# Kernel tuning notes

Measured on AMD Instinct MI355X. Metric: run time of the kernel, lower is better.

The kernel has to match this reference:

```python
import math
import jax, jax.numpy as jnp
import numpy as np

K = 64            # multiplicity per irrep
NE = 10           # num_elements
N_NODES = 10000
N_EDGES = 100000
AVG_NEIGH = 10.0
EDGE_DIM = 8
LS = [0, 1, 2]    # node/intermediate irreps 64x0e+64x1o+64x2e
LS_OUT = [0, 1]   # output irreps 64x0e+64x1o
INV_SQRT_K = 1.0 / math.sqrt(K)
MIX_NORM = 1.0 / math.sqrt(K * NE)

# ---- real spherical-harmonic Clebsch-Gordan coefficients (small l, exact) ----
def _cg(j1, m1, j2, m2, j3, m3):
    if m1 + m2 != m3 or not (abs(j1 - j2) <= j3 <= j1 + j2):
        return 0.0
    f = math.factorial
    pre = math.sqrt((2 * j3 + 1) * f(j1 + j2 - j3) * f(j1 - j2 + j3) * f(-j1 + j2 + j3) / f(j1 + j2 + j3 + 1))
    pre *= math.sqrt(f(j1 + m1) * f(j1 - m1) * f(j2 + m2) * f(j2 - m2) * f(j3 + m3) * f(j3 - m3))
    s = 0.0
    for k in range(j1 + j2 + j3 + 1):
        d = (j1 + j2 - j3 - k, j1 - m1 - k, j2 + m2 - k, j3 - j2 + m1 + k, j3 - j1 - m2 + k)
        if min(d) < 0:
            continue
        s += (-1) ** k / (f(k) * f(d[0]) * f(d[1]) * f(d[2]) * f(d[3]) * f(d[4]))
    return pre * s

def _u_real(l):
    # complex->real SH change of basis: Y_real = U @ Y_complex
    U = np.zeros((2 * l + 1, 2 * l + 1), dtype=np.complex128)
    U[l, l] = 1.0
    s = 1.0 / math.sqrt(2.0)
    for m in range(1, l + 1):
        U[l + m, l + m] = (-1) ** m * s
        U[l + m, l - m] = s
        U[l - m, l + m] = -1j * (-1) ** m * s
        U[l - m, l - m] = 1j * s
    return U

def real_cg(l1, l2, l3):
    C = np.zeros((2 * l1 + 1, 2 * l2 + 1, 2 * l3 + 1), dtype=np.complex128)
    for m1 in range(-l1, l1 + 1):
        for m2 in range(-l2, l2 + 1):
            m3 = m1 + m2
            if abs(m3) <= l3:
                C[l1 + m1, l2 + m2, l3 + m3] = _cg(l1, m1, l2, m2, l3, m3)
    U1, U2, U3 = _u_real(l1), _u_real(l2), _u_real(l3)
    Cr = np.einsum('ai,bj,ck,ijk->abc', U1, U2, U3.conj(), C)
    return np.ascontiguousarray(Cr.real).astype(np.float32)  # real since l1+l2+l3 even

# parity/triangle allowed paths (l1: edge sph, l2: node in, l3: intermediate) -> 11 paths
EDGE_PATHS = [(l1, l2, l3) for l1 in LS for l2 in LS for l3 in LS
              if abs(l1 - l2) <= l3 <= l1 + l2 and (l1 + l2 + l3) % 2 == 0]
N_EDGE_PATHS = len(EDGE_PATHS)  # 11
DEG2_PATHS = [(0, 0, 0), (1, 1, 0), (2, 2, 0), (0, 1, 1), (1, 2, 1)]
DEG3_PATHS = [(0, 0, 0), (1, 1, 0), (0, 1, 1), (1, 0, 1), (1, 2, 1)]
CG_EDGE = [real_cg(*p) for p in EDGE_PATHS]
CG_D2 = [real_cg(*p) for p in DEG2_PATHS]
CG_D3 = [real_cg(*p) for p in DEG3_PATHS]

def split_irreps(x, ls, mul):
    # ir_mul layout: per irrep a [(2l+1)*mul] flat segment, m index outer
    out, o = [], 0
    for l in ls:
        d = (2 * l + 1) * mul
        out.append(x[:, o:o + d].reshape(x.shape[0], 2 * l + 1, mul))
        o += d
    return out


def setup_inputs() -> dict:
    key = jax.random.key(0)
    ks = jax.random.split(key, 20)
    sender = jax.random.randint(ks[0], (N_EDGES,), 0, N_NODES)
    receiver = jax.random.randint(ks[1], (N_EDGES,), 0, N_NODES)
    indices = jax.random.randint(ks[2], (N_NODES,), 0, NE)
    node_attrs = jax.nn.one_hot(indices, NE, dtype=jnp.float32)
    node_feature_in = jax.random.normal(ks[3], (N_NODES, K * 9), dtype=jnp.float32)
    edge_length_embed = jax.random.normal(ks[4], (N_EDGES, EDGE_DIM), dtype=jnp.float32)
    edge_sph_embed = jax.random.normal(ks[5], (N_EDGES, 9), dtype=jnp.float32)
    W_lin_in = jax.random.normal(ks[6], (3, K, K), dtype=jnp.float32)
    mlp_W0 = jax.random.normal(ks[7], (EDGE_DIM, 32), dtype=jnp.float32) / math.sqrt(EDGE_DIM)
    mlp_b0 = jnp.zeros((32,), jnp.float32)
    mlp_W1 = jax.random.normal(ks[8], (32, 32), dtype=jnp.float32) / math.sqrt(32.0)
    mlp_b1 = jnp.zeros((32,), jnp.float32)
    mlp_W2 = jax.random.normal(ks[9], (32, 32), dtype=jnp.float32) / math.sqrt(32.0)
    mlp_b2 = jnp.zeros((32,), jnp.float32)
    mlp_W3 = jax.random.normal(ks[10], (32, N_EDGE_PATHS * K), dtype=jnp.float32) / math.sqrt(32.0)
    mlp_b3 = jnp.zeros((N_EDGE_PATHS * K,), jnp.float32)
    W_mix = jax.random.normal(ks[11], (3, NE, K, K), dtype=jnp.float32)
    w1 = jax.random.normal(ks[12], (NE, 2, K), dtype=jnp.float32)
    w2 = 0.1 * jax.random.normal(ks[13], (NE, len(DEG2_PATHS), K), dtype=jnp.float32)
    w3 = 0.05 * jax.random.normal(ks[14], (NE, len(DEG3_PATHS), K), dtype=jnp.float32)
    W_out_m = jax.random.normal(ks[15], (2, K, K), dtype=jnp.float32)
    W_out_h = jax.random.normal(ks[16], (2, K, K), dtype=jnp.float32)
    return dict(sender=sender, receiver=receiver, indices=indices, node_attrs=node_attrs,
                node_feature_in=node_feature_in, edge_length_embed=edge_length_embed,
                edge_sph_embed=edge_sph_embed, W_lin_in=W_lin_in,
                mlp_W0=mlp_W0, mlp_b0=mlp_b0, mlp_W1=mlp_W1, mlp_b1=mlp_b1,
                mlp_W2=mlp_W2, mlp_b2=mlp_b2, mlp_W3=mlp_W3, mlp_b3=mlp_b3,
                W_mix=W_mix, w1=w1, w2=w2, w3=w3, W_out_m=W_out_m, W_out_h=W_out_h)


def reference(sender, receiver, indices, node_attrs, node_feature_in,
              edge_length_embed, edge_sph_embed, W_lin_in,
              mlp_W0, mlp_b0, mlp_W1, mlp_b1, mlp_W2, mlp_b2, mlp_W3, mlp_b3,
              W_mix, w1, w2, w3, W_out_m, W_out_h):
    N = node_feature_in.shape[0]
    h1 = split_irreps(node_feature_in, LS, K)  # per-l [N, 2l+1, K]
    # ELinear_h1_2_h1p: per-irrep channel mixing
    h1p = [jnp.einsum('nmc,cd->nmd', h1[l], W_lin_in[l]) * INV_SQRT_K for l in LS]
    # residual radial MLP -> per-edge TP path weights [E, P, K]
    h = jax.nn.silu(edge_length_embed @ mlp_W0 + mlp_b0)
    h = h + jax.nn.silu(h @ mlp_W1 + mlp_b1)
    h = h + jax.nn.silu(h @ mlp_W2 + mlp_b2)
    Rl = (h @ mlp_W3 + mlp_b3).reshape(-1, N_EDGE_PATHS, K)
    sph = split_irreps(edge_sph_embed, LS, 1)  # per-l [E, 2l+1, 1]
    gx = [h1p[l][sender] for l in LS]          # gather sender node features
    # channelwise equivariant tensor product with per-edge radial weights
    msg = [None, None, None]
    for p, (l1, l2, l3) in enumerate(EDGE_PATHS):
        t = jnp.einsum('abd,ea,ebc->edc', jnp.asarray(CG_EDGE[p]), sph[l1][:, :, 0], gx[l2])
        t = t * Rl[:, p, None, :]
        msg[l3] = t if msg[l3] is None else msg[l3] + t
    # scatter-sum messages to receivers, normalized by avg num neighbors
    A = [jax.ops.segment_sum(msg[l], receiver, num_segments=N) / AVG_NEIGH for l in LS]
    # element-conditioned mixing (FCTP with num_elements x 0e attrs)
    Amix = [jnp.einsum('nmc,ne,ecd->nmd', A[l], node_attrs, W_mix[l]) * MIX_NORM for l in LS]
    # symmetric contraction (body order 3) with element-dependent channelwise weights
    w1n, w2n, w3n = w1[indices], w2[indices], w3[indices]
    T2 = [jnp.zeros_like(Amix[L]) for L in LS_OUT]
    for p, (l1, l2, L) in enumerate(DEG2_PATHS):
        t = jnp.einsum('abd,nac,nbc->ndc', jnp.asarray(CG_D2[p]), Amix[l1], Amix[l2])
        T2[L] = T2[L] + w2n[:, p, None, :] * t
    T3 = [jnp.zeros_like(Amix[L]) for L in LS_OUT]
    for q, (Lp, l3, L) in enumerate(DEG3_PATHS):
        t = jnp.einsum('abd,nac,nbc->ndc', jnp.asarray(CG_D3[q]), T2[Lp], Amix[l3])
        T3[L] = T3[L] + w3n[:, q, None, :] * t
    B = [w1n[:, L, None, :] * Amix[L] + T2[L] + T3[L] for L in LS_OUT]
    # node_feature_out = ELinear_h1_2_h2(h1) + ELinear_m2_2_h2(B)
    out = []
    for L in LS_OUT:
        y = jnp.einsum('nmc,cd->nmd', h1[L], W_out_h[L]) * INV_SQRT_K
        y = y + jnp.einsum('nmc,cd->nmd', B[L], W_out_m[L]) * INV_SQRT_K
        out.append(y.reshape(N, -1))
    return jnp.concatenate(out, axis=1)  # [N, 4K] = [N, 256]
```

## Files before the change

kernel.cpp:

```cpp
#include <hip/hip_runtime.h>
#include <math.h>

#define NNODES 10000
#define NEDGES 100000

typedef float v2f __attribute__((ext_vector_type(2)));

struct Cplx { double re, im; };

constexpr double cfact(int n){ double r=1.0; for(int i=2;i<=n;++i) r*=i; return r; }

constexpr double csqrt_(double x){
  if (x<=0.0) return 0.0;
  double g = x<1.0 ? 1.0 : x;
  for (int it=0; it<64; ++it){ double ng = 0.5*(g + x/g); if (ng==g) break; g = ng; }
  return g;
}

constexpr double cg_coeff(int j1,int m1,int j2,int m2,int j3,int m3){
  if (m1+m2!=m3) return 0.0;
  int lo = j1>j2 ? j1-j2 : j2-j1;
  if (j3<lo || j3>j1+j2) return 0.0;
  if (m1<-j1||m1>j1||m2<-j2||m2>j2||m3<-j3||m3>j3) return 0.0;
  double pre = csqrt_((2.0*j3+1.0)*cfact(j1+j2-j3)*cfact(j1-j2+j3)*cfact(-j1+j2+j3)/cfact(j1+j2+j3+1));
  pre *= csqrt_(cfact(j1+m1)*cfact(j1-m1)*cfact(j2+m2)*cfact(j2-m2)*cfact(j3+m3)*cfact(j3-m3));
  double s = 0.0;
  for (int k=0;k<=j1+j2+j3;++k){
    int d0=j1+j2-j3-k, d1=j1-m1-k, d2=j2+m2-k, d3=j3-j2+m1+k, d4=j3-j1-m2+k;
    if (d0<0||d1<0||d2<0||d3<0||d4<0) continue;
    double term = 1.0/(cfact(k)*cfact(d0)*cfact(d1)*cfact(d2)*cfact(d3)*cfact(d4));
    s += (k&1) ? -term : term;
  }
  return pre*s;
}

constexpr Cplx uent(int l,int a,int i){
  const double s = 0.70710678118654752440;
  int ma = a - l;
  if (ma==0) { if (i==l) return Cplx{1.0,0.0}; return Cplx{0.0,0.0}; }
  if (ma>0){
    int m = ma; double sg = (m&1) ? -1.0 : 1.0;
    if (i==l+m) return Cplx{sg*s, 0.0};
    if (i==l-m) return Cplx{s, 0.0};
    return Cplx{0.0,0.0};
  }
  int m = -ma; double sg = (m&1) ? -1.0 : 1.0;
  if (i==l+m) return Cplx{0.0, -sg*s};
  if (i==l-m) return Cplx{0.0, s};
  return Cplx{0.0,0.0};
}

constexpr double real_cg_entry(int l1,int l2,int l3,int a,int b,int c){
  double acc = 0.0;
  int ii0 = a, ii1 = 2*l1-a;
  int jj0 = b, jj1 = 2*l2-b;
  for (int x=0;x<2;++x){
    int i = (x==0)? ii0 : ii1;
    if (x==1 && ii1==ii0) break;
    Cplx u1 = uent(l1,a,i); if (u1.re==0.0 && u1.im==0.0) continue;
    for (int y=0;y<2;++y){
      int j = (y==0)? jj0 : jj1;
      if (y==1 && jj1==jj0) break;
      Cplx u2 = uent(l2,b,j); if (u2.re==0.0 && u2.im==0.0) continue;
      int k = (i-l1)+(j-l2)+l3;
      if (k<0 || k>2*l3) continue;
      Cplx u3 = uent(l3,c,k); if (u3.re==0.0 && u3.im==0.0) continue;
      double cg = cg_coeff(l1,i-l1,l2,j-l2,l3,k-l3);
      if (cg==0.0) continue;
      double pr = u1.re*u2.re - u1.im*u2.im;
      double pi = u1.re*u2.im + u1.im*u2.re;
      acc += (pr*u3.re + pi*u3.im) * cg;
    }
  }
  return acc;
}

struct CGT { float v[5][5][5]; };
constexpr CGT make_cg(int l1,int l2,int l3){
  CGT t{};
  for (int a=0;a<2*l1+1;++a)
    for (int b=0;b<2*l2+1;++b)
      for (int c=0;c<2*l3+1;++c)
        t.v[a][b][c] = (float)real_cg_entry(l1,l2,l3,a,b,c);
  return t;
}

__device__ __forceinline__ float silu_(float x){ return x / (1.0f + __expf(-x)); }

union H16 { _Float16 h; unsigned short u; };
__device__ __forceinline__ float h2f(unsigned short u){ H16 c; c.u = u; return (float)c.h; }
__device__ __forceinline__ unsigned int pack2(float a, float b){
  H16 x, y; x.h = (_Float16)a; y.h = (_Float16)b;
  return ((unsigned int)y.u << 16) | x.u;
}
__device__ __forceinline__ v2f make2(float s){ v2f r; r.x = s; r.y = s; return r; }

template<int L1,int L2,int L3>
__device__ __forceinline__ void tp_pk(const v2f* sp, const v2f* g, v2f rl, v2f* msg){
  constexpr CGT T = make_cg(L1,L2,L3);
  constexpr int NA = 2*L1+1, NB = 2*L2+1, ND = 2*L3+1;
  v2f t[ND];
#pragma unroll
  for (int d=0;d<ND;++d) t[d] = make2(0.f);
#pragma unroll
  for (int b=0;b<NB;++b){
#pragma unroll
    for (int d=0;d<ND;++d){
      v2f u = make2(0.f); bool any = false;
#pragma unroll
      for (int a=0;a<NA;++a){
        const float cg = T.v[a][b][d];
        if (cg != 0.f){ u = cg*sp[a] + u; any = true; }
      }
      if (any) t[d] = u*g[b] + t[d];
    }
  }
#pragma unroll
  for (int d=0;d<ND;++d) msg[d] = rl*t[d] + msg[d];
}

template<int L1,int L2,int L3>
__device__ __forceinline__ void sc_accum(const float* X, const float* Y, float w, float* out){
  constexpr CGT T = make_cg(L1,L2,L3);
  constexpr int NA = 2*L1+1, NB = 2*L2+1, ND = 2*L3+1;
#pragma unroll
  for (int d=0;d<ND;++d){
    float s = 0.f;
#pragma unroll
    for (int a=0;a<NA;++a){
#pragma unroll
      for (int b=0;b<NB;++b){
        const float cg = T.v[a][b][d];
        if (cg != 0.f) s = fmaf(cg*X[a], Y[b], s);
      }
    }
    out[d] = fmaf(w, s, out[d]);
  }
}

__global__ void __launch_bounds__(64) k_lin_in(const float* __restrict__ h1,
                                               const float* __restrict__ W,
                                               float* __restrict__ h1p,
                                               int* __restrict__ deg){
  const int n = blockIdx.x;
  const int d = threadIdx.x;
  if (d == 0) deg[n] = 0;
  const float* row = h1 + (long)n*576;
  float acc[9];
#pragma unroll
  for (int i=0;i<9;++i) acc[i] = 0.f;
  for (int c=0;c<64;++c){
    const float w0 = W[c*64 + d];
    const float w1 = W[4096 + c*64 + d];
    const float w2 = W[8192 + c*64 + d];
    acc[0] = fmaf(row[c], w0, acc[0]);
#pragma unroll
    for (int m=0;m<3;++m) acc[1+m] = fmaf(row[64+m*64+c], w1, acc[1+m]);
#pragma unroll
    for (int m=0;m<5;++m) acc[4+m] = fmaf(row[256+m*64+c], w2, acc[4+m]);
  }
  float* o = h1p + (long)n*576;
  o[d] = acc[0]*0.125f;
#pragma unroll
  for (int m=0;m<3;++m) o[64+m*64+d] = acc[1+m]*0.125f;
#pragma unroll
  for (int m=0;m<5;++m) o[256+m*64+d] = acc[4+m]*0.125f;
}

__global__ void __launch_bounds__(256) k_mlp(const float* __restrict__ ele,
                                             const float* __restrict__ W0, const float* __restrict__ b0,
                                             const float* __restrict__ W1, const float* __restrict__ b1,
                                             const float* __restrict__ W2, const float* __restrict__ b2,
                                             float* __restrict__ hmlp){
  const int e = blockIdx.x*256 + threadIdx.x;
  if (e >= NEDGES) return;
  float x[8];
#pragma unroll
  for (int i=0;i<8;++i) x[i] = ele[(long)e*8 + i];
  float h[32];
#pragma unroll
  for (int d=0;d<32;++d){
    float acc = b0[d];
#pragma unroll
    for (int i=0;i<8;++i) acc = fmaf(x[i], W0[i*32+d], acc);
    h[d] = silu_(acc);
  }
#pragma unroll
  for (int L=0; L<2; ++L){
    const float* Wl = L ? W2 : W1;
    const float* bl = L ? b2 : b1;
    float acc[32];
#pragma unroll
    for (int d=0;d<32;++d) acc[d] = bl[d];
    for (int j=0;j<32;++j){
      const float hj = h[j];
#pragma unroll
      for (int d=0;d<32;++d) acc[d] = fmaf(hj, Wl[j*32+d], acc[d]);
    }
#pragma unroll
    for (int d=0;d<32;++d) h[d] += silu_(acc[d]);
  }
  float* o = hmlp + (long)e*32;
#pragma unroll
  for (int d=0;d<32;++d) o[d] = h[d];
}

__global__ void __launch_bounds__(256) k_hist(const int* __restrict__ receiver, int* __restrict__ deg){
  const int e = blockIdx.x*256 + threadIdx.x;
  if (e < NEDGES) atomicAdd(&deg[receiver[e]], 1);
}

__global__ void __launch_bounds__(256) k_scan(const int* __restrict__ deg,
                                              int* __restrict__ rowptr,
                                              int* __restrict__ cursor){
  __shared__ int sums[256];
  const int t = threadIdx.x;
  const int CH = 40;
  const int base = t*CH;
  int s = 0;
  for (int i=0;i<CH;++i){ int idx = base+i; if (idx < NNODES) s += deg[idx]; }
  sums[t] = s; __syncthreads();
  for (int off=1; off<256; off<<=1){
    int v = (t>=off) ? sums[t-off] : 0;
    __syncthreads();
    sums[t] += v;
    __syncthreads();
  }
  int run = (t==0) ? 0 : sums[t-1];
  for (int i=0;i<CH;++i){
    int idx = base+i;
    if (idx < NNODES){ rowptr[idx] = run; cursor[idx] = run; run += deg[idx]; }
  }
  if (t==255) rowptr[NNODES] = sums[255];
}

__global__ void __launch_bounds__(256) k_fill_pos(const int* __restrict__ receiver,
                                                  int* __restrict__ cursor,
                                                  int* __restrict__ epos){
  const int e = blockIdx.x*256 + threadIdx.x;
  if (e < NEDGES) epos[e] = atomicAdd(&cursor[receiver[e]], 1);
}

__global__ void __launch_bounds__(256) k_edge_pk(const int* __restrict__ sender,
                                             const int* __restrict__ epos,
                                             const float* __restrict__ hmlp,
                                             const float* __restrict__ sph,
                                             const float* __restrict__ h1p,
                                             const float* __restrict__ W3, const float* __restrict__ b3,
                                             unsigned int* __restrict__ msg){
  __shared__ float sps[4][72];
  const int wid  = threadIdx.x >> 6;
  const int lane = threadIdx.x & 63;
  const int ubase = __builtin_amdgcn_readfirstlane((blockIdx.x*4 + wid) * 8);

  {
    const int idx = lane;
    const int e = idx/9, a = idx - 9*e;
    sps[wid][a*8 + e] = sph[(long)ubase*9 + idx];
  }
  if (lane < 8){
    const int idx = 64 + lane;
    const int e = idx/9, a = idx - 9*e;
    sps[wid][a*8 + e] = sph[(long)ubase*9 + idx];
  }

  int sidx[8], pos[8];
#pragma unroll
  for (int e=0;e<8;++e){ sidx[e] = sender[ubase+e]; pos[e] = epos[ubase+e]; }

  v2f g2[4][9];
#pragma unroll
  for (int q=0;q<4;++q){
    const float* hp0 = h1p + (long)sidx[2*q]  *576;
    const float* hp1 = h1p + (long)sidx[2*q+1]*576;
#pragma unroll
    for (int i=0;i<9;++i){ g2[q][i].x = hp0[i*64+lane]; g2[q][i].y = hp1[i*64+lane]; }
  }
#pragma unroll
  for (int q=0;q<4;++q)
#pragma unroll
    for (int i=0;i<9;++i) asm volatile("" : "+v"(g2[q][i]));

  const float* hu = hmlp + (long)ubase*32;

  v2f rl2[11][4];
#pragma unroll
  for (int p=0;p<11;++p){
    const float bb = b3[p*64+lane];
#pragma unroll
    for (int q=0;q<4;++q) rl2[p][q] = make2(bb);
  }
  for (int jb=0;jb<32;jb+=4){
    float w3v[4][11];
#pragma unroll
    for (int jj=0;jj<4;++jj)
#pragma unroll
      for (int p=0;p<11;++p)
        w3v[jj][p] = W3[(jb+jj)*704 + p*64 + lane];
#pragma unroll
    for (int q=0;q<4;++q){
#pragma unroll
      for (int jj=0;jj<4;++jj){
        v2f h2; h2.x = hu[(2*q)*32 + jb + jj]; h2.y = hu[(2*q+1)*32 + jb + jj];
#pragma unroll
        for (int p=0;p<11;++p) rl2[p][q] = h2*w3v[jj][p] + rl2[p][q];
      }
    }
  }

#pragma unroll
  for (int q=0;q<4;++q){
    v2f sp2[9];
#pragma unroll
    for (int a=0;a<9;++a) sp2[a] = *(const v2f*)&sps[wid][a*8 + 2*q];
    v2f m0[1]; m0[0] = make2(0.f);
    v2f m1[3]; m1[0]=m1[1]=m1[2]=make2(0.f);
    v2f m2[5]; m2[0]=m2[1]=m2[2]=m2[3]=m2[4]=make2(0.f);
    tp_pk<0,0,0>(sp2+0, &g2[q][0], rl2[0][q],  m0);
    tp_pk<0,1,1>(sp2+0, &g2[q][1], rl2[1][q],  m1);
    tp_pk<0,2,2>(sp2+0, &g2[q][4], rl2[2][q],  m2);
    tp_pk<1,0,1>(sp2+1, &g2[q][0], rl2[3][q],  m1);
    tp_pk<1,1,0>(sp2+1, &g2[q][1], rl2[4][q],  m0);
    tp_pk<1,1,2>(sp2+1, &g2[q][1], rl2[5][q],  m2);
    tp_pk<1,2,1>(sp2+1, &g2[q][4], rl2[6][q],  m1);
    tp_pk<2,0,2>(sp2+4, &g2[q][0], rl2[7][q],  m2);
    tp_pk<2,1,1>(sp2+4, &g2[q][1], rl2[8][q],  m1);
    tp_pk<2,2,0>(sp2+4, &g2[q][4], rl2[9][q],  m0);
    tp_pk<2,2,2>(sp2+4, &g2[q][4], rl2[10][q], m2);
    {
      unsigned int pk[5];
      pk[0] = pack2(m0[0].x, m1[0].x);
      pk[1] = pack2(m1[1].x, m1[2].x);
      pk[2] = pack2(m2[0].x, m2[1].x);
      pk[3] = pack2(m2[2].x, m2[3].x);
      pk[4] = pack2(m2[4].x, 0.f);
      unsigned int* mp = msg + (size_t)pos[2*q]*320;
#pragma unroll
      for (int k=0;k<5;++k) mp[k*64 + lane] = pk[k];
    }
    {
      unsigned int pk[5];
      pk[0] = pack2(m0[0].y, m1[0].y);
      pk[1] = pack2(m1[1].y, m1[2].y);
      pk[2] = pack2(m2[0].y, m2[1].y);
      pk[3] = pack2(m2[2].y, m2[3].y);
      pk[4] = pack2(m2[4].y, 0.f);
      unsigned int* mp = msg + (size_t)pos[2*q+1]*320;
#pragma unroll
      for (int k=0;k<5;++k) mp[k*64 + lane] = pk[k];
    }
  }
}

__global__ void __launch_bounds__(256) k_node_c(const int* __restrict__ indices,
                                             const float* __restrict__ h1,
                                             const int* __restrict__ rowptr,
                                             const unsigned int* __restrict__ msg,
                                             const float* __restrict__ Wmix,
                                             const float* __restrict__ w1,
                                             const float* __restrict__ w2,
                                             const float* __restrict__ w3,
                                             const float* __restrict__ Wom,
                                             const float* __restrict__ Woh,
                                             float* __restrict__ out){
  __shared__ float S[4][9][64];
  __shared__ float Bb[4][4][64];
  const int wid  = threadIdx.x >> 6;
  const int lane = threadIdx.x & 63;
  const int n = blockIdx.x*4 + wid;
  const int e = __builtin_amdgcn_readfirstlane(indices[n]);

  {
    const int start = rowptr[n], end = rowptr[n+1];
    float A[9];
#pragma unroll
    for (int i=0;i<9;++i) A[i] = 0.f;
    for (int q=start; q<end; ++q){
      const unsigned int* mp = msg + (size_t)q*320;
#pragma unroll
      for (int k=0;k<5;++k){
        const unsigned int v = mp[k*64 + lane];
        A[2*k] += h2f((unsigned short)(v & 0xffff));
        if (2*k+1 < 9) A[2*k+1] += h2f((unsigned short)(v >> 16));
      }
    }
#pragma unroll
    for (int i=0;i<9;++i) S[wid][i][lane] = A[i];
  }

  float ax[9];
#pragma unroll
  for (int i=0;i<9;++i) ax[i] = 0.f;
  {
    const float* Wm0 = Wmix + (size_t)(0*10 + e)*4096;
    const float* Wm1 = Wmix + (size_t)(1*10 + e)*4096;
    const float* Wm2 = Wmix + (size_t)(2*10 + e)*4096;
    for (int c=0;c<64;++c){
      const float wv0 = Wm0[c*64+lane];
      const float wv1 = Wm1[c*64+lane];
      const float wv2 = Wm2[c*64+lane];
      ax[0] = fmaf(S[wid][0][c], wv0, ax[0]);
#pragma unroll
      for (int m=0;m<3;++m) ax[1+m] = fmaf(S[wid][1+m][c], wv1, ax[1+m]);
#pragma unroll
      for (int m=0;m<5;++m) ax[4+m] = fmaf(S[wid][4+m][c], wv2, ax[4+m]);
    }
  }
#pragma unroll
  for (int i=0;i<9;++i) ax[i] *= 0.0039528470752104741f;

  const float* amix0 = ax;
  const float* amix1 = ax+1;
  const float* amix2 = ax+4;
  float w2n[5], w3n[5];
#pragma unroll
  for (int p=0;p<5;++p){
    w2n[p] = w2[(size_t)(e*5+p)*64 + lane];
    w3n[p] = w3[(size_t)(e*5+p)*64 + lane];
  }
  float t20[1] = {0.f}, t21[3] = {0.f,0.f,0.f};
  sc_accum<0,0,0>(amix0, amix0, w2n[0], t20);
  sc_accum<1,1,0>(amix1, amix1, w2n[1], t20);
  sc_accum<2,2,0>(amix2, amix2, w2n[2], t20);
  sc_accum<0,1,1>(amix0, amix1, w2n[3], t21);
  sc_accum<1,2,1>(amix1, amix2, w2n[4], t21);
  float t30[1] = {0.f}, t31[3] = {0.f,0.f,0.f};
  sc_accum<0,0,0>(t20, amix0, w3n[0], t30);
  sc_accum<1,1,0>(t21, amix1, w3n[1], t30);
  sc_accum<0,1,1>(t20, amix1, w3n[2], t31);
  sc_accum<1,0,1>(t21, amix0, w3n[3], t31);
  sc_accum<1,2,1>(t21, amix2, w3n[4], t31);

  const float w1_0 = w1[(size_t)(e*2+0)*64 + lane];
  const float w1_1 = w1[(size_t)(e*2+1)*64 + lane];
  Bb[wid][0][lane] = fmaf(w1_0, amix0[0], t20[0] + t30[0]);
#pragma unroll
  for (int m=0;m<3;++m) Bb[wid][1+m][lane] = fmaf(w1_1, amix1[m], t21[m] + t31[m]);

  {
    const float* hrow = h1 + (long)n*576;
#pragma unroll
    for (int r=0;r<9;++r) S[wid][r][lane] = hrow[r*64 + lane];
  }

  float o[4];
#pragma unroll
  for (int i=0;i<4;++i) o[i] = 0.f;
  for (int c=0;c<64;++c){
    const float wh0 = Woh[c*64+lane];
    const float wh1 = Woh[4096 + c*64+lane];
    const float wm0 = Wom[c*64+lane];
    const float wm1 = Wom[4096 + c*64+lane];
    o[0] = fmaf(S[wid][0][c], wh0, o[0]);
    o[0] = fmaf(Bb[wid][0][c], wm0, o[0]);
#pragma unroll
    for (int m=0;m<3;++m){
      o[1+m] = fmaf(S[wid][1+m][c], wh1, o[1+m]);
      o[1+m] = fmaf(Bb[wid][1+m][c], wm1, o[1+m]);
    }
  }
  float* orow = out + (long)n*256;
  orow[lane] = o[0]*0.125f;
#pragma unroll
  for (int m=0;m<3;++m) orow[64+m*64+lane] = o[1+m]*0.125f;
}

extern "C" void kernel_launch(void* const* d_in, const int* in_sizes, int n_in,
                              void* d_out, int out_size, void* d_ws, size_t ws_size,
                              hipStream_t stream){
  const int*   sender   = (const int*)  d_in[0];
  const int*   receiver = (const int*)  d_in[1];
  const int*   indices  = (const int*)  d_in[2];
  const float* node_feat= (const float*)d_in[4];
  const float* ele      = (const float*)d_in[5];
  const float* sph      = (const float*)d_in[6];
  const float* W_lin    = (const float*)d_in[7];
  const float* W0 = (const float*)d_in[8],  *b0 = (const float*)d_in[9];
  const float* W1 = (const float*)d_in[10], *b1 = (const float*)d_in[11];
  const float* W2 = (const float*)d_in[12], *b2 = (const float*)d_in[13];
  const float* W3 = (const float*)d_in[14], *b3 = (const float*)d_in[15];
  const float* Wmix = (const float*)d_in[16];
  const float* w1 = (const float*)d_in[17];
  const float* w2 = (const float*)d_in[18];
  const float* w3 = (const float*)d_in[19];
  const float* Wom = (const float*)d_in[20];
  const float* Woh = (const float*)d_in[21];
  float* out = (float*)d_out;

  char* ws = (char*)d_ws;
  const size_t OFF_H1P  = 0;
  const size_t OFF_HMLP = OFF_H1P  + (size_t)NNODES*576*4;
  const size_t OFF_MSG  = OFF_HMLP + (size_t)NEDGES*32*4;
  const size_t OFF_DEG  = OFF_MSG  + (size_t)NEDGES*320*4;
  const size_t OFF_ROW  = OFF_DEG  + 40960;
  const size_t OFF_CUR  = OFF_ROW  + 40960;
  const size_t OFF_EPOS = OFF_CUR  + 40960;

  float* h1p  = (float*)(ws + OFF_H1P);
  float* hmlp = (float*)(ws + OFF_HMLP);
  unsigned int* msg = (unsigned int*)(ws + OFF_MSG);
  int* deg    = (int*)(ws + OFF_DEG);
  int* rowptr = (int*)(ws + OFF_ROW);
  int* cursor = (int*)(ws + OFF_CUR);
  int* epos   = (int*)(ws + OFF_EPOS);

  k_lin_in<<<NNODES, 64, 0, stream>>>(node_feat, W_lin, h1p, deg);
  k_mlp<<<(NEDGES+255)/256, 256, 0, stream>>>(ele, W0,b0,W1,b1,W2,b2, hmlp);
  k_hist<<<(NEDGES+255)/256, 256, 0, stream>>>(receiver, deg);
  k_scan<<<1, 256, 0, stream>>>(deg, rowptr, cursor);
  k_fill_pos<<<(NEDGES+255)/256, 256, 0, stream>>>(receiver, cursor, epos);
  k_edge_pk<<<NEDGES/32, 256, 0, stream>>>(sender, epos, hmlp, sph, h1p, W3, b3, msg);
  k_node_c<<<NNODES/4, 256, 0, stream>>>(indices, node_feat, rowptr, msg,
                                         Wmix, w1, w2, w3, Wom, Woh, out);
}
```

Baseline: 258.0 us.

## Sort nodes by element and process two nodes per wave with packed math

Adds a single-block counting sort of nodes by element type, then rewrites the node kernel so each wavefront handles two nodes with packed v2f arithmetic. When both nodes share an element, one set of mixing weights serves both. The change also folds the degree histogram into the MLP kernel, retiles the input linear kernel to four nodes per block, and swaps the asm register barrier in the edge kernel for s_setprio. The cost is an extra serial sort launch, a divergent branch for mixed-element pairs, and doubled shared memory.

```diff
diff --git a/kernel.cpp b/kernel.cpp
--- a/kernel.cpp
+++ b/kernel.cpp
@@ -3,6 +3,7 @@
 
 #define NNODES 10000
 #define NEDGES 100000
+#define NE 10
 
 typedef float v2f __attribute__((ext_vector_type(2)));
 
@@ -120,31 +121,47 @@
 }
 
 template<int L1,int L2,int L3>
-__device__ __forceinline__ void sc_accum(const float* X, const float* Y, float w, float* out){
+__device__ __forceinline__ void sc_pk(const v2f* X, const v2f* Y, v2f w, v2f* out){
   constexpr CGT T = make_cg(L1,L2,L3);
   constexpr int NA = 2*L1+1, NB = 2*L2+1, ND = 2*L3+1;
 #pragma unroll
   for (int d=0;d<ND;++d){
-    float s = 0.f;
+    v2f s = make2(0.f);
 #pragma unroll
     for (int a=0;a<NA;++a){
 #pragma unroll
       for (int b=0;b<NB;++b){
         const float cg = T.v[a][b][d];
-        if (cg != 0.f) s = fmaf(cg*X[a], Y[b], s);
+        if (cg != 0.f) s = (cg*X[a])*Y[b] + s;
       }
     }
-    out[d] = fmaf(w, s, out[d]);
-  }
-}
-
-__global__ void __launch_bounds__(64) k_lin_in(const float* __restrict__ h1,
+    out[d] = w*s + out[d];
+  }
+}
+
+__global__ void __launch_bounds__(1024) k_nodesort(const int* __restrict__ idx,
+                                                   int* __restrict__ nperm){
+  __shared__ int cnt[NE];
+  __shared__ int base[NE];
+  const int t = threadIdx.x;
+  if (t < NE) cnt[t] = 0;
+  __syncthreads();
+  for (int n=t; n<NNODES; n+=1024) atomicAdd(&cnt[idx[n]], 1);
+  __syncthreads();
+  if (t == 0){ int run=0; for (int e=0;e<NE;++e){ base[e]=run; run+=cnt[e]; } }
+  __syncthreads();
+  if (t < NE) cnt[t] = base[t];
+  __syncthreads();
+  for (int n=t; n<NNODES; n+=1024){ int p = atomicAdd(&cnt[idx[n]],1); nperm[p]=n; }
+}
+
+__global__ void __launch_bounds__(256) k_lin_in(const float* __restrict__ h1,
                                                const float* __restrict__ W,
                                                float* __restrict__ h1p,
-                                               int* __restrict__ deg){
-  const int n = blockIdx.x;
-  const int d = threadIdx.x;
-  if (d == 0) deg[n] = 0;
+                                               int* __restrict__ rdeg){
+  const int n = blockIdx.x*4 + (threadIdx.x>>6);
+  const int d = threadIdx.x & 63;
+  if (d == 0) rdeg[n] = 0;
   const float* row = h1 + (long)n*576;
   float acc[9];
 #pragma unroll
@@ -171,9 +188,12 @@
                                              const float* __restrict__ W0, const float* __restrict__ b0,
                                              const float* __restrict__ W1, const float* __restrict__ b1,
                                              const float* __restrict__ W2, const float* __restrict__ b2,
+                                             const int* __restrict__ receiver,
+                                             int* __restrict__ rdeg,
                                              float* __restrict__ hmlp){
   const int e = blockIdx.x*256 + threadIdx.x;
   if (e >= NEDGES) return;
+  atomicAdd(&rdeg[receiver[e]], 1);
   float x[8];
 #pragma unroll
   for (int i=0;i<8;++i) x[i] = ele[(long)e*8 + i];
@@ -203,11 +223,6 @@
   float* o = hmlp + (long)e*32;
 #pragma unroll
   for (int d=0;d<32;++d) o[d] = h[d];
-}
-
-__global__ void __launch_bounds__(256) k_hist(const int* __restrict__ receiver, int* __restrict__ deg){
-  const int e = blockIdx.x*256 + threadIdx.x;
-  if (e < NEDGES) atomicAdd(&deg[receiver[e]], 1);
 }
 
 __global__ void __launch_bounds__(256) k_scan(const int* __restrict__ deg,
@@ -276,12 +291,10 @@
 #pragma unroll
     for (int i=0;i<9;++i){ g2[q][i].x = hp0[i*64+lane]; g2[q][i].y = hp1[i*64+lane]; }
   }
-#pragma unroll
-  for (int q=0;q<4;++q)
-#pragma unroll
-    for (int i=0;i<9;++i) asm volatile("" : "+v"(g2[q][i]));
 
   const float* hu = hmlp + (long)ubase*32;
+
+  __builtin_amdgcn_s_setprio(1);
 
   v2f rl2[11][4];
 #pragma unroll
@@ -350,9 +363,11 @@
       for (int k=0;k<5;++k) mp[k*64 + lane] = pk[k];
     }
   }
-}
-
-__global__ void __launch_bounds__(256) k_node_c(const int* __restrict__ indices,
+  __builtin_amdgcn_s_setprio(0);
+}
+
+__global__ void __launch_bounds__(256) k_node_p(const int* __restrict__ indices,
+                                             const int* __restrict__ nperm,
                                              const float* __restrict__ h1,
                                              const int* __restrict__ rowptr,
                                              const unsigned int* __restrict__ msg,
@@ -363,15 +378,20 @@
                                              const float* __restrict__ Wom,
                                              const float* __restrict__ Woh,
                                              float* __restrict__ out){
-  __shared__ float S[4][9][64];
-  __shared__ float Bb[4][4][64];
+  __shared__ float S[4][9][64][2];
+  __shared__ float Bb[4][4][64][2];
   const int wid  = threadIdx.x >> 6;
   const int lane = threadIdx.x & 63;
-  const int n = blockIdx.x*4 + wid;
-  const int e = __builtin_amdgcn_readfirstlane(indices[n]);
-
-  {
-    const int start = rowptr[n], end = rowptr[n+1];
+  const int p0 = (blockIdx.x*4 + wid)*2;
+  const int n0 = __builtin_amdgcn_readfirstlane(nperm[p0]);
+  const int n1 = __builtin_amdgcn_readfirstlane(nperm[p0+1]);
+  const int e0 = __builtin_amdgcn_readfirstlane(indices[n0]);
+  const int e1 = __builtin_amdgcn_readfirstlane(indices[n1]);
+
+#pragma unroll
+  for (int k2=0;k2<2;++k2){
+    const int nk = k2 ? n1 : n0;
+    const int start = rowptr[nk], end = rowptr[nk+1];
     float A[9];
 #pragma unroll
     for (int i=0;i<9;++i) A[i] = 0.f;
@@ -385,84 +405,118 @@
       }
     }
 #pragma unroll
-    for (int i=0;i<9;++i) S[wid][i][lane] = A[i];
-  }
-
-  float ax[9];
-#pragma unroll
-  for (int i=0;i<9;++i) ax[i] = 0.f;
-  {
-    const float* Wm0 = Wmix + (size_t)(0*10 + e)*4096;
-    const float* Wm1 = Wmix + (size_t)(1*10 + e)*4096;
-    const float* Wm2 = Wmix + (size_t)(2*10 + e)*4096;
+    for (int i=0;i<9;++i) S[wid][i][lane][k2] = A[i];
+  }
+
+  v2f ax[9];
+#pragma unroll
+  for (int i=0;i<9;++i) ax[i] = make2(0.f);
+  if (e0 == e1){
+    const float* Wm0 = Wmix + (size_t)(0*NE + e0)*4096;
+    const float* Wm1 = Wmix + (size_t)(1*NE + e0)*4096;
+    const float* Wm2 = Wmix + (size_t)(2*NE + e0)*4096;
     for (int c=0;c<64;++c){
       const float wv0 = Wm0[c*64+lane];
       const float wv1 = Wm1[c*64+lane];
       const float wv2 = Wm2[c*64+lane];
-      ax[0] = fmaf(S[wid][0][c], wv0, ax[0]);
-#pragma unroll
-      for (int m=0;m<3;++m) ax[1+m] = fmaf(S[wid][1+m][c], wv1, ax[1+m]);
-#pragma unroll
-      for (int m=0;m<5;++m) ax[4+m] = fmaf(S[wid][4+m][c], wv2, ax[4+m]);
-    }
-  }
-#pragma unroll
-  for (int i=0;i<9;++i) ax[i] *= 0.0039528470752104741f;
-
-  const float* amix0 = ax;
-  const float* amix1 = ax+1;
-  const float* amix2 = ax+4;
-  float w2n[5], w3n[5];
+      ax[0] = (*(const v2f*)&S[wid][0][c][0])*wv0 + ax[0];
+#pragma unroll
+      for (int m=0;m<3;++m) ax[1+m] = (*(const v2f*)&S[wid][1+m][c][0])*wv1 + ax[1+m];
+#pragma unroll
+      for (int m=0;m<5;++m) ax[4+m] = (*(const v2f*)&S[wid][4+m][c][0])*wv2 + ax[4+m];
+    }
+  } else {
+    const float* Wm0a = Wmix + (size_t)(0*NE + e0)*4096;
+    const float* Wm1a = Wmix + (size_t)(1*NE + e0)*4096;
+    const float* Wm2a = Wmix + (size_t)(2*NE + e0)*4096;
+    const float* Wm0b = Wmix + (size_t)(0*NE + e1)*4096;
+    const float* Wm1b = Wmix + (size_t)(1*NE + e1)*4096;
+    const float* Wm2b = Wmix + (size_t)(2*NE + e1)*4096;
+    for (int c=0;c<64;++c){
+      v2f wv0; wv0.x = Wm0a[c*64+lane]; wv0.y = Wm0b[c*64+lane];
+      v2f wv1; wv1.x = Wm1a[c*64+lane]; wv1.y = Wm1b[c*64+lane];
+      v2f wv2; wv2.x = Wm2a[c*64+lane]; wv2.y = Wm2b[c*64+lane];
+      ax[0] = (*(const v2f*)&S[wid][0][c][0])*wv0 + ax[0];
+#pragma unroll
+      for (int m=0;m<3;++m) ax[1+m] = (*(const v2f*)&S[wid][1+m][c][0])*wv1 + ax[1+m];
+#pragma unroll
+      for (int m=0;m<5;++m) ax[4+m] = (*(const v2f*)&S[wid][4+m][c][0])*wv2 + ax[4+m];
+    }
+  }
+#pragma unroll
+  for (int i=0;i<9;++i) ax[i] = ax[i]*0.0039528470752104741f;
+
+  const v2f* amix0 = ax;
+  const v2f* amix1 = ax+1;
+  const v2f* amix2 = ax+4;
+  v2f w2n[5], w3n[5];
 #pragma unroll
   for (int p=0;p<5;++p){
-    w2n[p] = w2[(size_t)(e*5+p)*64 + lane];
-    w3n[p] = w3[(size_t)(e*5+p)*64 + lane];
-  }
-  float t20[1] = {0.f}, t21[3] = {0.f,0.f,0.f};
-  sc_accum<0,0,0>(amix0, amix0, w2n[0], t20);
-  sc_accum<1,1,0>(amix1, amix1, w2n[1], t20);
-  sc_accum<2,2,0>(amix2, amix2, w2n[2], t20);
-  sc_accum<0,1,1>(amix0, amix1, w2n[3], t21);
-  sc_accum<1,2,1>(amix1, amix2, w2n[4], t21);
-  float t30[1] = {0.f}, t31[3] = {0.f,0.f,0.f};
-  sc_accum<0,0,0>(t20, amix0, w3n[0], t30);
-  sc_accum<1,1,0>(t21, amix1, w3n[1], t30);
-  sc_accum<0,1,1>(t20, amix1, w3n[2], t31);
-  sc_accum<1,0,1>(t21, amix0, w3n[3], t31);
-  sc_accum<1,2,1>(t21, amix2, w3n[4], t31);
-
-  const float w1_0 = w1[(size_t)(e*2+0)*64 + lane];
-  const float w1_1 = w1[(size_t)(e*2+1)*64 + lane];
-  Bb[wid][0][lane] = fmaf(w1_0, amix0[0], t20[0] + t30[0]);
-#pragma unroll
-  for (int m=0;m<3;++m) Bb[wid][1+m][lane] = fmaf(w1_1, amix1[m], t21[m] + t31[m]);
+    w2n[p].x = w2[(size_t)(e0*5+p)*64 + lane];
+    w2n[p].y = w2[(size_t)(e1*5+p)*64 + lane];
+    w3n[p].x = w3[(size_t)(e0*5+p)*64 + lane];
+    w3n[p].y = w3[(size_t)(e1*5+p)*64 + lane];
+  }
+  v2f t20[1]; t20[0] = make2(0.f);
+  v2f t21[3]; t21[0]=t21[1]=t21[2]=make2(0.f);
+  sc_pk<0,0,0>(amix0, amix0, w2n[0], t20);
+  sc_pk<1,1,0>(amix1, amix1, w2n[1], t20);
+  sc_pk<2,2,0>(amix2, amix2, w2n[2], t20);
+  sc_pk<0,1,1>(amix0, amix1, w2n[3], t21);
+  sc_pk<1,2,1>(amix1, amix2, w2n[4], t21);
+  v2f t30[1]; t30[0] = make2(0.f);
+  v2f t31[3]; t31[0]=t31[1]=t31[2]=make2(0.f);
+  sc_pk<0,0,0>(t20, amix0, w3n[0], t30);
+  sc_pk<1,1,0>(t21, amix1, w3n[1], t30);
+  sc_pk<0,1,1>(t20, amix1, w3n[2], t31);
+  sc_pk<1,0,1>(t21, amix0, w3n[3], t31);
+  sc_pk<1,2,1>(t21, amix2, w3n[4], t31);
+
+  v2f w1_0, w1_1;
+  w1_0.x = w1[(size_t)(e0*2+0)*64 + lane];
+  w1_0.y = w1[(size_t)(e1*2+0)*64 + lane];
+  w1_1.x = w1[(size_t)(e0*2+1)*64 + lane];
+  w1_1.y = w1[(size_t)(e1*2+1)*64 + lane];
+  *(v2f*)&Bb[wid][0][lane][0] = w1_0*amix0[0] + (t20[0] + t30[0]);
+#pragma unroll
+  for (int m=0;m<3;++m)
+    *(v2f*)&Bb[wid][1+m][lane][0] = w1_1*amix1[m] + (t21[m] + t31[m]);
 
   {
-    const float* hrow = h1 + (long)n*576;
-#pragma unroll
-    for (int r=0;r<9;++r) S[wid][r][lane] = hrow[r*64 + lane];
-  }
-
-  float o[4];
-#pragma unroll
-  for (int i=0;i<4;++i) o[i] = 0.f;
+    const float* hr0 = h1 + (long)n0*576;
+    const float* hr1 = h1 + (long)n1*576;
+#pragma unroll
+    for (int r=0;r<4;++r){
+      S[wid][r][lane][0] = hr0[r*64 + lane];
+      S[wid][r][lane][1] = hr1[r*64 + lane];
+    }
+  }
+
+  v2f o[4];
+#pragma unroll
+  for (int i=0;i<4;++i) o[i] = make2(0.f);
   for (int c=0;c<64;++c){
     const float wh0 = Woh[c*64+lane];
     const float wh1 = Woh[4096 + c*64+lane];
     const float wm0 = Wom[c*64+lane];
     const float wm1 = Wom[4096 + c*64+lane];
-    o[0] = fmaf(S[wid][0][c], wh0, o[0]);
-    o[0] = fmaf(Bb[wid][0][c], wm0, o[0]);
+    o[0] = (*(const v2f*)&S[wid][0][c][0])*wh0 + o[0];
+    o[0] = (*(const v2f*)&Bb[wid][0][c][0])*wm0 + o[0];
 #pragma unroll
     for (int m=0;m<3;++m){
-      o[1+m] = fmaf(S[wid][1+m][c], wh1, o[1+m]);
-      o[1+m] = fmaf(Bb[wid][1+m][c], wm1, o[1+m]);
-    }
-  }
-  float* orow = out + (long)n*256;
-  orow[lane] = o[0]*0.125f;
-#pragma unroll
-  for (int m=0;m<3;++m) orow[64+m*64+lane] = o[1+m]*0.125f;
+      o[1+m] = (*(const v2f*)&S[wid][1+m][c][0])*wh1 + o[1+m];
+      o[1+m] = (*(const v2f*)&Bb[wid][1+m][c][0])*wm1 + o[1+m];
+    }
+  }
+  float* or0 = out + (long)n0*256;
+  float* or1 = out + (long)n1*256;
+  or0[lane] = o[0].x*0.125f;
+  or1[lane] = o[0].y*0.125f;
+#pragma unroll
+  for (int m=0;m<3;++m){
+    or0[64+m*64+lane] = o[1+m].x*0.125f;
+    or1[64+m*64+lane] = o[1+m].y*0.125f;
+  }
 }
 
 extern "C" void kernel_launch(void* const* d_in, const int* in_sizes, int n_in,
@@ -491,25 +545,28 @@
   const size_t OFF_H1P  = 0;
   const size_t OFF_HMLP = OFF_H1P  + (size_t)NNODES*576*4;
   const size_t OFF_MSG  = OFF_HMLP + (size_t)NEDGES*32*4;
-  const size_t OFF_DEG  = OFF_MSG  + (size_t)NEDGES*320*4;
-  const size_t OFF_ROW  = OFF_DEG  + 40960;
-  const size_t OFF_CUR  = OFF_ROW  + 40960;
-  const size_t OFF_EPOS = OFF_CUR  + 40960;
+  const size_t OFF_RDEG = OFF_MSG  + (size_t)NEDGES*320*4;
+  const size_t OFF_RROW = OFF_RDEG + 40960;
+  const size_t OFF_RCUR = OFF_RROW + 40964;
+  const size_t OFF_EPOS = OFF_RCUR + 40960;
+  const size_t OFF_NPRM = OFF_EPOS + (size_t)NEDGES*4;
 
   float* h1p  = (float*)(ws + OFF_H1P);
   float* hmlp = (float*)(ws + OFF_HMLP);
   unsigned int* msg = (unsigned int*)(ws + OFF_MSG);
-  int* deg    = (int*)(ws + OFF_DEG);
-  int* rowptr = (int*)(ws + OFF_ROW);
-  int* cursor = (int*)(ws + OFF_CUR);
+  int* rdeg   = (int*)(ws + OFF_RDEG);
+  int* rrow   = (int*)(ws + OFF_RROW);
+  int* rcur   = (int*)(ws + OFF_RCUR);
   int* epos   = (int*)(ws + OFF_EPOS);
-
-  k_lin_in<<<NNODES, 64, 0, stream>>>(node_feat, W_lin, h1p, deg);
-  k_mlp<<<(NEDGES+255)/256, 256, 0, stream>>>(ele, W0,b0,W1,b1,W2,b2, hmlp);
-  k_hist<<<(NEDGES+255)/256, 256, 0, stream>>>(receiver, deg);
-  k_scan<<<1, 256, 0, stream>>>(deg, rowptr, cursor);
-  k_fill_pos<<<(NEDGES+255)/256, 256, 0, stream>>>(receiver, cursor, epos);
+  int* nperm  = (int*)(ws + OFF_NPRM);
+
+  k_nodesort<<<1, 1024, 0, stream>>>(indices, nperm);
+  k_lin_in<<<NNODES/4, 256, 0, stream>>>(node_feat, W_lin, h1p, rdeg);
+  k_mlp<<<(NEDGES+255)/256, 256, 0, stream>>>(ele, W0,b0,W1,b1,W2,b2,
+                                              receiver, rdeg, hmlp);
+  k_scan<<<1, 256, 0, stream>>>(rdeg, rrow, rcur);
+  k_fill_pos<<<(NEDGES+255)/256, 256, 0, stream>>>(receiver, rcur, epos);
   k_edge_pk<<<NEDGES/32, 256, 0, stream>>>(sender, epos, hmlp, sph, h1p, W3, b3, msg);
-  k_node_c<<<NNODES/4, 256, 0, stream>>>(indices, node_feat, rowptr, msg,
+  k_node_p<<<NNODES/8, 256, 0, stream>>>(indices, nperm, node_feat, rrow, msg,
                                          Wmix, w1, w2, w3, Wom, Woh, out);
 }
```

Measured after the change: 278.3 us. 7.9% more time.
